# Optimization experiments

Measured on AMD Instinct MI355X. Metric: run time of the kernel, lower is better.

The kernel has to match this reference:

```python
import jax, jax.numpy as jnp
import numpy as np

LPC_ORDER = 24  # M; k has last dim M+1


def setup_inputs() -> dict:
    key = jax.random.key(0)
    k = jax.random.normal(key, (2097152, LPC_ORDER + 1), dtype=jnp.float32)
    return {"k": k}


def reference(k) -> jnp.ndarray:
    # PARCOR -> LPC Levinson recursion.
    # a = k.clone(); for m in 2..M: a[1:m] += k[m] * flip(a[1:m])
    # Note: a[..., m] is never written before step m, so k[..., m] == a[..., m].
    M = k.shape[-1] - 1
    a = k
    for m in range(2, M + 1):  # small static loop over coefficient order
        am = a[..., 1:m]
        km = k[..., m:m + 1]
        a = a.at[..., 1:m].set(am + km * am[..., ::-1])
    return a
```

## Files before the change

### kernel.cpp

```cpp
#include <hip/hip_runtime.h>

#define ORDER 24
#define W 25
#define ROWS_PER_BLOCK 256
#define THREADS 256
#define WAVE_FLOATS (64 * W)

__device__ __forceinline__ void levinson(float* __restrict__ a)
{
    #pragma unroll
    for (int m = 2; m <= ORDER; ++m) {
        const float km = a[m];
        #pragma unroll
        for (int j = 1; j <= (m - 1) / 2; ++j) {
            const float lo = a[j], hi = a[m - j];
            a[j]     = fmaf(km, hi, lo);
            a[m - j] = fmaf(km, lo, hi);
        }
        if ((m & 1) == 0) {
            const float v = a[m / 2];
            a[m / 2] = fmaf(km, v, v);
        }
    }
}

__global__ __launch_bounds__(THREADS)
void parcor2lpc_kernel(const float* __restrict__ in,
                       float* __restrict__ out, int rows)
{
    __shared__ __align__(16) float lds[ROWS_PER_BLOCK * W];

    const int t    = threadIdx.x;
    const int wave = t >> 6;
    const int lane = t & 63;
    const long long row0 = (long long)blockIdx.x * ROWS_PER_BLOCK;
    const long long base = row0 * W;
    const long long rem  = (long long)rows - row0;
    const int nrows = rem >= ROWS_PER_BLOCK ? ROWS_PER_BLOCK : (int)rem;

    if (nrows == ROWS_PER_BLOCK) {
        const int wbase = wave * WAVE_FLOATS;
        const float* __restrict__ gw = in + base + wbase;

        #pragma unroll
        for (int k = 0; k < 6; ++k) {
            __builtin_amdgcn_global_load_lds(
                (const __attribute__((address_space(1))) void*)(gw + k * 256 + lane * 4),
                (__attribute__((address_space(3))) void*)(&lds[wbase + k * 256]),
                16, 0, 0);
        }
        __builtin_amdgcn_global_load_lds(
            (const __attribute__((address_space(1))) void*)(gw + 1536 + lane),
            (__attribute__((address_space(3))) void*)(&lds[wbase + 1536]),
            4, 0, 0);

        asm volatile("s_waitcnt vmcnt(0)" ::: "memory");

        float a[W];
        #pragma unroll
        for (int j = 0; j < W; ++j) a[j] = lds[t * W + j];

        levinson(a);

        #pragma unroll
        for (int j = 0; j < W; ++j) lds[t * W + j] = a[j];

        float4* __restrict__ gout = (float4*)(out + base);
        const float4* sv = (const float4*)lds;
        const int f0 = wave * (WAVE_FLOATS / 4);
        #pragma unroll
        for (int k = 0; k < 6; ++k)
            gout[f0 + k * 64 + lane] = sv[f0 + k * 64 + lane];
        if (lane < 16)
            gout[f0 + 384 + lane] = sv[f0 + 384 + lane];
    } else {
        for (int i = t; i < nrows * W; i += THREADS)
            lds[i] = in[base + i];
        __syncthreads();
        if (t < nrows) {
            float a[W];
            for (int j = 0; j < W; ++j) a[j] = lds[t * W + j];
            levinson(a);
            for (int j = 0; j < W; ++j) lds[t * W + j] = a[j];
        }
        __syncthreads();
        for (int i = t; i < nrows * W; i += THREADS)
            out[base + i] = lds[i];
    }
}

extern "C" void kernel_launch(void* const* d_in, const int* in_sizes, int n_in,
                              void* d_out, int out_size, void* d_ws, size_t ws_size,
                              hipStream_t stream) {
    const float* k = (const float*)d_in[0];
    float* out = (float*)d_out;
    const int rows = in_sizes[0] / W;
    const int grid = (rows + ROWS_PER_BLOCK - 1) / ROWS_PER_BLOCK;
    parcor2lpc_kernel<<<grid, THREADS, 0, stream>>>(k, out, rows);
}
```

Measured before the change: 341.2 us.

## Double-buffer two row chunks per block to overlap DMA with Levinson compute

Each block now handles two 256-row chunks. It issues async global-to-LDS loads for both chunks up front, then waits only for the first chunk (vmcnt(7)) before starting the recursion on it, so the second chunk's load overlaps that compute. The cost being targeted is the stall between load and compute inside a block. In exchange, each block uses twice the LDS (about 50KB), which may lower occupancy and weaken the overlap the GPU already gets from running many blocks at once.

```diff
diff --git a/kernel.cpp b/kernel.cpp
--- a/kernel.cpp
+++ b/kernel.cpp
@@ -2,7 +2,7 @@
 
 #define ORDER 24
 #define W 25
-#define ROWS_PER_BLOCK 256
+#define CHUNK_ROWS 256
 #define THREADS 256
 #define WAVE_FLOATS (64 * W)
 
@@ -24,68 +24,103 @@
     }
 }
 
+__device__ __forceinline__ void dma_wave_slice(const float* __restrict__ g,
+                                               float* __restrict__ l, int lane)
+{
+    #pragma unroll
+    for (int k = 0; k < 6; ++k)
+        __builtin_amdgcn_global_load_lds(
+            (const __attribute__((address_space(1))) void*)(g + k * 256 + lane * 4),
+            (__attribute__((address_space(3))) void*)(l + k * 256), 16, 0, 0);
+    __builtin_amdgcn_global_load_lds(
+        (const __attribute__((address_space(1))) void*)(g + 1536 + lane),
+        (__attribute__((address_space(3))) void*)(l + 1536), 4, 0, 0);
+}
+
 __global__ __launch_bounds__(THREADS)
 void parcor2lpc_kernel(const float* __restrict__ in,
                        float* __restrict__ out, int rows)
 {
-    __shared__ __align__(16) float lds[ROWS_PER_BLOCK * W];
+    __shared__ __align__(16) float lds[2][CHUNK_ROWS * W];
 
     const int t    = threadIdx.x;
     const int wave = t >> 6;
     const int lane = t & 63;
-    const long long row0 = (long long)blockIdx.x * ROWS_PER_BLOCK;
-    const long long base = row0 * W;
-    const long long rem  = (long long)rows - row0;
-    const int nrows = rem >= ROWS_PER_BLOCK ? ROWS_PER_BLOCK : (int)rem;
 
-    if (nrows == ROWS_PER_BLOCK) {
-        const int wbase = wave * WAVE_FLOATS;
-        const float* __restrict__ gw = in + base + wbase;
+    const long long c0    = (long long)blockIdx.x * 2;
+    const long long row00 = c0 * CHUNK_ROWS;
+    const long long rem0  = (long long)rows - row00;
 
-        #pragma unroll
-        for (int k = 0; k < 6; ++k) {
-            __builtin_amdgcn_global_load_lds(
-                (const __attribute__((address_space(1))) void*)(gw + k * 256 + lane * 4),
-                (__attribute__((address_space(3))) void*)(&lds[wbase + k * 256]),
-                16, 0, 0);
+    if (rem0 >= 2 * CHUNK_ROWS) {
+        const int wb = wave * WAVE_FLOATS;
+        const float* g0 = in + row00 * W + wb;
+        const float* g1 = g0 + CHUNK_ROWS * W;
+
+        dma_wave_slice(g0, &lds[0][wb], lane);
+        dma_wave_slice(g1, &lds[1][wb], lane);
+
+        asm volatile("s_waitcnt vmcnt(7)" ::: "memory");
+
+        {
+            float a[W];
+            #pragma unroll
+            for (int j = 0; j < W; ++j) a[j] = lds[0][t * W + j];
+            levinson(a);
+            #pragma unroll
+            for (int j = 0; j < W; ++j) lds[0][t * W + j] = a[j];
         }
-        __builtin_amdgcn_global_load_lds(
-            (const __attribute__((address_space(1))) void*)(gw + 1536 + lane),
-            (__attribute__((address_space(3))) void*)(&lds[wbase + 1536]),
-            4, 0, 0);
 
         asm volatile("s_waitcnt vmcnt(0)" ::: "memory");
 
-        float a[W];
-        #pragma unroll
-        for (int j = 0; j < W; ++j) a[j] = lds[t * W + j];
+        {
+            float4* __restrict__ gout = (float4*)(out + row00 * W);
+            const float4* sv = (const float4*)&lds[0][0];
+            const int f0 = wave * (WAVE_FLOATS / 4);
+            #pragma unroll
+            for (int k = 0; k < 6; ++k)
+                gout[f0 + k * 64 + lane] = sv[f0 + k * 64 + lane];
+            if (lane < 16)
+                gout[f0 + 384 + lane] = sv[f0 + 384 + lane];
+        }
+        {
+            float a[W];
+            #pragma unroll
+            for (int j = 0; j < W; ++j) a[j] = lds[1][t * W + j];
+            levinson(a);
+            #pragma unroll
+            for (int j = 0; j < W; ++j) lds[1][t * W + j] = a[j];
 
-        levinson(a);
-
-        #pragma unroll
-        for (int j = 0; j < W; ++j) lds[t * W + j] = a[j];
-
-        float4* __restrict__ gout = (float4*)(out + base);
-        const float4* sv = (const float4*)lds;
-        const int f0 = wave * (WAVE_FLOATS / 4);
-        #pragma unroll
-        for (int k = 0; k < 6; ++k)
-            gout[f0 + k * 64 + lane] = sv[f0 + k * 64 + lane];
-        if (lane < 16)
-            gout[f0 + 384 + lane] = sv[f0 + 384 + lane];
+            float4* __restrict__ gout = (float4*)(out + (row00 + CHUNK_ROWS) * W);
+            const float4* sv = (const float4*)&lds[1][0];
+            const int f0 = wave * (WAVE_FLOATS / 4);
+            #pragma unroll
+            for (int k = 0; k < 6; ++k)
+                gout[f0 + k * 64 + lane] = sv[f0 + k * 64 + lane];
+            if (lane < 16)
+                gout[f0 + 384 + lane] = sv[f0 + 384 + lane];
+        }
     } else {
-        for (int i = t; i < nrows * W; i += THREADS)
-            lds[i] = in[base + i];
-        __syncthreads();
-        if (t < nrows) {
-            float a[W];
-            for (int j = 0; j < W; ++j) a[j] = lds[t * W + j];
-            levinson(a);
-            for (int j = 0; j < W; ++j) lds[t * W + j] = a[j];
+        for (int c = 0; c < 2; ++c) {
+            const long long row0 = (c0 + c) * CHUNK_ROWS;
+            const long long rem  = (long long)rows - row0;
+            if (rem <= 0) break;
+            const int nrows = rem >= CHUNK_ROWS ? CHUNK_ROWS : (int)rem;
+            const long long base = row0 * W;
+            float* buf = lds[c];
+            for (int i = t; i < nrows * W; i += THREADS)
+                buf[i] = in[base + i];
+            __syncthreads();
+            if (t < nrows) {
+                float a[W];
+                for (int j = 0; j < W; ++j) a[j] = buf[t * W + j];
+                levinson(a);
+                for (int j = 0; j < W; ++j) buf[t * W + j] = a[j];
+            }
+            __syncthreads();
+            for (int i = t; i < nrows * W; i += THREADS)
+                out[base + i] = buf[i];
+            __syncthreads();
         }
-        __syncthreads();
-        for (int i = t; i < nrows * W; i += THREADS)
-            out[base + i] = lds[i];
     }
 }
 
@@ -95,6 +130,7 @@
     const float* k = (const float*)d_in[0];
     float* out = (float*)d_out;
     const int rows = in_sizes[0] / W;
-    const int grid = (rows + ROWS_PER_BLOCK - 1) / ROWS_PER_BLOCK;
+    const int chunks = (rows + CHUNK_ROWS - 1) / CHUNK_ROWS;
+    const int grid = (chunks + 1) / 2;
     parcor2lpc_kernel<<<grid, THREADS, 0, stream>>>(k, out, rows);
 }
```

Measured after the change: 341.8 us. Within noise of the previous version (+0.2%).
